# Kernel tuning notes

Hardware: AMD Instinct MI355X
Metric: run time of the kernel (lower is better)

## Reference

```python
import jax, jax.numpy as jnp
import numpy as np

# Uniform per-graph sizes (static shapes for jit):
B, M, P = 32, 40, 400          # graphs, ligand atoms/graph, protein nodes/graph
H, HEADS = 64, 8               # hid_dim, heads
E = B * M * P                  # total bipartite pairs = 512000


def _make_indices():
    """Replicates create_index() for uniform sizes: per-graph cartesian product."""
    g = np.arange(B, dtype=np.int64)
    # mol atom j of graph i repeated P times
    mol_index = np.repeat(np.arange(B * M, dtype=np.int64), P)
    # protein indices [i*P, (i+1)*P) tiled M times within each graph
    pro_index = (g[:, None, None] * P
                 + np.zeros((M, 1), dtype=np.int64)
                 + np.arange(P, dtype=np.int64)[None, None, :]).reshape(-1)
    mol_batch = np.repeat(g, M)   # create_batch(mol_size)
    return mol_index, pro_index, mol_batch


def setup_inputs() -> dict:
    key = jax.random.key(0)
    ks = jax.random.split(key, 8)
    mol_index, pro_index, mol_batch = _make_indices()
    s = 1.0 / np.sqrt(2 * H)
    return {
        "mol_feats": jax.random.normal(ks[0], (B * M, H), jnp.float32),
        "pro_feats": jax.random.normal(ks[1], (B * P, H), jnp.float32),
        "spatial_feats": jax.random.normal(ks[2], (B * P, H), jnp.float32),
        "mol_index": jnp.asarray(mol_index),
        "pro_index": jnp.asarray(pro_index),
        "mol_batch": jnp.asarray(mol_batch),
        "W_sigma": jax.random.normal(ks[3], (2 * H, HEADS), jnp.float32) * s,
        "b_sigma": jnp.zeros((HEADS,), jnp.float32),
        "W_mu": jax.random.normal(ks[4], (2 * H, HEADS), jnp.float32) * s,
        "b_mu": jnp.zeros((HEADS,), jnp.float32),
        "W1": jax.random.normal(ks[5], (HEADS, 2 * HEADS), jnp.float32) / np.sqrt(HEADS),
        "b1": jnp.zeros((2 * HEADS,), jnp.float32),
        "W2": jax.random.normal(ks[6], (2 * HEADS, 1), jnp.float32) / np.sqrt(2 * HEADS),
        "b2": jnp.zeros((1,), jnp.float32),
    }


def reference(mol_feats, pro_feats, spatial_feats, mol_index, pro_index, mol_batch,
              W_sigma, b_sigma, W_mu, b_mu, W1, b1, W2, b2):
    n_mol = mol_feats.shape[0]
    pro = pro_feats * spatial_feats                                  # [Np, H]
    # bipartite gather -> [E, 2H]
    atom_pairs = jnp.concatenate([mol_feats[mol_index], pro[pro_index]], axis=-1)
    sigma = jax.nn.elu(atom_pairs @ W_sigma + b_sigma) + 1.1         # [E, heads]
    mu = jax.nn.elu(atom_pairs @ W_mu + b_mu) + 1.0                  # [E, heads]
    # scatter_sum over mol atoms, then over graphs
    y = jax.ops.segment_sum(mu, mol_index, num_segments=n_mol)       # [Nm, heads]
    y = jax.ops.segment_sum(y, mol_batch, num_segments=B) * 0.001    # [B, heads]
    y = jax.nn.elu(y @ W1 + b1)
    y_pred = y @ W2 + b2                                             # [B, 1]
    return (mu, sigma, y_pred)
```

## Files before the change

### kernel.cpp

```cpp
#include <hip/hip_runtime.h>
#include <math.h>

#define B_   32
#define M_   40
#define P_   400
#define H_   64
#define HEADS_ 8
#define NMOL (B_ * M_)
#define NPRO (B_ * P_)
#define EPG  (M_ * P_)
#define E_   (B_ * EPG)
#define CHUNKS 63

__device__ __forceinline__ float elu_f(float x) {
    return x > 0.0f ? x : expm1f(x);
}

__global__ void precompute_kernel(const float* __restrict__ mol_feats,
                                  const float* __restrict__ pro_feats,
                                  const float* __restrict__ spatial,
                                  const float* __restrict__ Ws,
                                  const float* __restrict__ Wm,
                                  float* __restrict__ Amol_s, float* __restrict__ Amol_m,
                                  float* __restrict__ Apro_s, float* __restrict__ Apro_m)
{
    __shared__ float Wlds[2][128 * HEADS_];
    for (int i = threadIdx.x; i < 128 * HEADS_; i += 256) {
        Wlds[0][i] = Ws[i];
        Wlds[1][i] = Wm[i];
    }
    __syncthreads();

    const int o = threadIdx.x & 15;
    const int sel = o >> 3;
    const int h = o & 7;
    const int row = blockIdx.x * 16 + (threadIdx.x >> 4);
    if (row >= NMOL + NPRO) return;

    float acc = 0.0f;
    if (row < NMOL) {
        const float* f = mol_feats + row * H_;
        const float* w = &Wlds[sel][0 * HEADS_ + h];
        #pragma unroll
        for (int k = 0; k < H_; ++k) acc += f[k] * w[k * HEADS_];
        (sel ? Amol_m : Amol_s)[row * HEADS_ + h] = acc;
    } else {
        const int pr = row - NMOL;
        const float* pf = pro_feats + pr * H_;
        const float* sf = spatial   + pr * H_;
        const float* w = &Wlds[sel][H_ * HEADS_ + h];
        #pragma unroll
        for (int k = 0; k < H_; ++k) acc += pf[k] * sf[k] * w[k * HEADS_];
        (sel ? Apro_m : Apro_s)[pr * HEADS_ + h] = acc;
    }
}

__global__ void pair_kernel(const float* __restrict__ Amol_s, const float* __restrict__ Amol_m,
                            const float* __restrict__ Apro_s, const float* __restrict__ Apro_m,
                            const float* __restrict__ b_s, const float* __restrict__ b_m,
                            float* __restrict__ out_mu, float* __restrict__ out_sigma,
                            float* __restrict__ partials)
{
    const int g = blockIdx.x / CHUNKS;
    const int chunk = blockIdx.x - g * CHUNKS;
    const int el = chunk * 256 + threadIdx.x;

    float mu[HEADS_];
    #pragma unroll
    for (int h = 0; h < HEADS_; ++h) mu[h] = 0.0f;

    if (el < EPG) {
        const unsigned mr = (unsigned)el / P_;
        const unsigned p  = (unsigned)el - mr * P_;
        const int e = g * EPG + el;
        const int molrow = g * M_ + (int)mr;
        const int prorow = g * P_ + (int)p;

        const float4* ams = (const float4*)(Amol_s + molrow * HEADS_);
        const float4* amm = (const float4*)(Amol_m + molrow * HEADS_);
        const float4* aps = (const float4*)(Apro_s + prorow * HEADS_);
        const float4* apm = (const float4*)(Apro_m + prorow * HEADS_);

        float as[HEADS_], am[HEADS_];
        {
            float4 a0 = ams[0], a1 = ams[1], p0 = aps[0], p1 = aps[1];
            as[0]=a0.x+p0.x; as[1]=a0.y+p0.y; as[2]=a0.z+p0.z; as[3]=a0.w+p0.w;
            as[4]=a1.x+p1.x; as[5]=a1.y+p1.y; as[6]=a1.z+p1.z; as[7]=a1.w+p1.w;
        }
        {
            float4 a0 = amm[0], a1 = amm[1], p0 = apm[0], p1 = apm[1];
            am[0]=a0.x+p0.x; am[1]=a0.y+p0.y; am[2]=a0.z+p0.z; am[3]=a0.w+p0.w;
            am[4]=a1.x+p1.x; am[5]=a1.y+p1.y; am[6]=a1.z+p1.z; am[7]=a1.w+p1.w;
        }

        float sig[HEADS_];
        #pragma unroll
        for (int h = 0; h < HEADS_; ++h) {
            sig[h] = elu_f(as[h] + b_s[h]) + 1.1f;
            mu[h]  = elu_f(am[h] + b_m[h]) + 1.0f;
        }

        float4* oms = (float4*)(out_sigma + (size_t)e * HEADS_);
        float4* omm = (float4*)(out_mu    + (size_t)e * HEADS_);
        oms[0] = make_float4(sig[0], sig[1], sig[2], sig[3]);
        oms[1] = make_float4(sig[4], sig[5], sig[6], sig[7]);
        omm[0] = make_float4(mu[0], mu[1], mu[2], mu[3]);
        omm[1] = make_float4(mu[4], mu[5], mu[6], mu[7]);
    }

    const int lane = threadIdx.x & 63;
    const int wave = threadIdx.x >> 6;
    #pragma unroll
    for (int off = 32; off >= 1; off >>= 1) {
        #pragma unroll
        for (int h = 0; h < HEADS_; ++h)
            mu[h] += __shfl_down(mu[h], off, 64);
    }
    __shared__ float red[4][HEADS_];
    if (lane == 0) {
        #pragma unroll
        for (int h = 0; h < HEADS_; ++h) red[wave][h] = mu[h];
    }
    __syncthreads();
    if (threadIdx.x < HEADS_) {
        const int h = threadIdx.x;
        float s = red[0][h] + red[1][h] + red[2][h] + red[3][h];
        partials[(size_t)blockIdx.x * HEADS_ + h] = s;
    }
}

__global__ void final_kernel(const float* __restrict__ partials,
                             const float* __restrict__ W1, const float* __restrict__ b1,
                             const float* __restrict__ W2, const float* __restrict__ b2,
                             float* __restrict__ y_out)
{
    __shared__ float ys[B_][HEADS_];
    const int g = threadIdx.x >> 3;
    const int h = threadIdx.x & 7;
    if (g < B_) {
        float s = 0.0f;
        for (int c = 0; c < CHUNKS; ++c)
            s += partials[((size_t)g * CHUNKS + c) * HEADS_ + h];
        ys[g][h] = s * 0.001f;
    }
    __syncthreads();
    if (threadIdx.x < B_) {
        const int gg = threadIdx.x;
        float acc = b2[0];
        #pragma unroll
        for (int j = 0; j < 2 * HEADS_; ++j) {
            float hj = b1[j];
            #pragma unroll
            for (int k = 0; k < HEADS_; ++k)
                hj += ys[gg][k] * W1[k * (2 * HEADS_) + j];
            acc += elu_f(hj) * W2[j];
        }
        y_out[gg] = acc;
    }
}

extern "C" void kernel_launch(void* const* d_in, const int* in_sizes, int n_in,
                              void* d_out, int out_size, void* d_ws, size_t ws_size,
                              hipStream_t stream) {
    const float* mol_feats = (const float*)d_in[0];
    const float* pro_feats = (const float*)d_in[1];
    const float* spatial   = (const float*)d_in[2];
    const float* W_sigma = (const float*)d_in[6];
    const float* b_sigma = (const float*)d_in[7];
    const float* W_mu    = (const float*)d_in[8];
    const float* b_mu    = (const float*)d_in[9];
    const float* W1      = (const float*)d_in[10];
    const float* b1      = (const float*)d_in[11];
    const float* W2      = (const float*)d_in[12];
    const float* b2      = (const float*)d_in[13];

    float* out = (float*)d_out;
    float* out_mu    = out;
    float* out_sigma = out + (size_t)E_ * HEADS_;
    float* y_out     = out + 2 * (size_t)E_ * HEADS_;

    float* ws = (float*)d_ws;
    float* Amol_s = ws;
    float* Amol_m = Amol_s + NMOL * HEADS_;
    float* Apro_s = Amol_m + NMOL * HEADS_;
    float* Apro_m = Apro_s + NPRO * HEADS_;
    float* partials = Apro_m + NPRO * HEADS_;

    {
        const int rows = NMOL + NPRO;
        const int blocks = (rows + 15) / 16;
        precompute_kernel<<<blocks, 256, 0, stream>>>(
            mol_feats, pro_feats, spatial, W_sigma, W_mu,
            Amol_s, Amol_m, Apro_s, Apro_m);
    }
    pair_kernel<<<B_ * CHUNKS, 256, 0, stream>>>(
        Amol_s, Amol_m, Apro_s, Apro_m, b_sigma, b_mu,
        out_mu, out_sigma, partials);
    final_kernel<<<1, 256, 0, stream>>>(partials, W1, b1, W2, b2, y_out);
}
```

Measured before the change: 29.49 us.

## Process two pairs per thread, use exp2 ELU, vectorize precompute loads

The pair kernel now has each thread handle two consecutive pairs. This halves the block count and reuses the molecule-row loads and bias registers across both pairs. ELU uses exp2f in place of expm1f, with the +1 folded into the constant. The precompute kernel reads features as float4, and the final reduction loop is unrolled for the new chunk count. The cost is a strided store pattern across threads (each thread writes two adjacent 32-byte records), which may reduce store coalescing, and slightly less precision in ELU for small negative inputs.

```diff
diff --git a/kernel.cpp b/kernel.cpp
--- a/kernel.cpp
+++ b/kernel.cpp
@@ -10,10 +10,15 @@
 #define NPRO (B_ * P_)
 #define EPG  (M_ * P_)
 #define E_   (B_ * EPG)
-#define CHUNKS 63
+#define PPT  2
+#define BLOCK_PAIRS (256 * PPT)
+#define CHUNKS 32
+#define NBLK (B_ * CHUNKS)
+
+#define LOG2E 1.4426950408889634f
 
 __device__ __forceinline__ float elu_f(float x) {
-    return x > 0.0f ? x : expm1f(x);
+    return x > 0.0f ? x : exp2f(x * LOG2E) - 1.0f;
 }
 
 __global__ void precompute_kernel(const float* __restrict__ mol_feats,
@@ -39,18 +44,31 @@
 
     float acc = 0.0f;
     if (row < NMOL) {
-        const float* f = mol_feats + row * H_;
-        const float* w = &Wlds[sel][0 * HEADS_ + h];
-        #pragma unroll
-        for (int k = 0; k < H_; ++k) acc += f[k] * w[k * HEADS_];
+        const float4* f4 = (const float4*)(mol_feats + (size_t)row * H_);
+        const float* w = &Wlds[sel][h];
+        #pragma unroll
+        for (int kk = 0; kk < 16; ++kk) {
+            float4 v = f4[kk];
+            acc += v.x * w[(4 * kk + 0) * HEADS_]
+                 + v.y * w[(4 * kk + 1) * HEADS_]
+                 + v.z * w[(4 * kk + 2) * HEADS_]
+                 + v.w * w[(4 * kk + 3) * HEADS_];
+        }
         (sel ? Amol_m : Amol_s)[row * HEADS_ + h] = acc;
     } else {
         const int pr = row - NMOL;
-        const float* pf = pro_feats + pr * H_;
-        const float* sf = spatial   + pr * H_;
+        const float4* f4 = (const float4*)(pro_feats + (size_t)pr * H_);
+        const float4* s4 = (const float4*)(spatial   + (size_t)pr * H_);
         const float* w = &Wlds[sel][H_ * HEADS_ + h];
         #pragma unroll
-        for (int k = 0; k < H_; ++k) acc += pf[k] * sf[k] * w[k * HEADS_];
+        for (int kk = 0; kk < 16; ++kk) {
+            float4 v = f4[kk];
+            float4 s = s4[kk];
+            acc += (v.x * s.x) * w[(4 * kk + 0) * HEADS_]
+                 + (v.y * s.y) * w[(4 * kk + 1) * HEADS_]
+                 + (v.z * s.z) * w[(4 * kk + 2) * HEADS_]
+                 + (v.w * s.w) * w[(4 * kk + 3) * HEADS_];
+        }
         (sel ? Apro_m : Apro_s)[pr * HEADS_ + h] = acc;
     }
 }
@@ -61,71 +79,97 @@
                             float* __restrict__ out_mu, float* __restrict__ out_sigma,
                             float* __restrict__ partials)
 {
-    const int g = blockIdx.x / CHUNKS;
-    const int chunk = blockIdx.x - g * CHUNKS;
-    const int el = chunk * 256 + threadIdx.x;
-
-    float mu[HEADS_];
+    const int g = blockIdx.x >> 5;
+    const int chunk = blockIdx.x & 31;
+    const int t = threadIdx.x;
+
+    float bs[HEADS_], bm[HEADS_];
+    {
+        const float4* b4 = (const float4*)b_s;
+        float4 x0 = b4[0], x1 = b4[1];
+        bs[0]=x0.x; bs[1]=x0.y; bs[2]=x0.z; bs[3]=x0.w;
+        bs[4]=x1.x; bs[5]=x1.y; bs[6]=x1.z; bs[7]=x1.w;
+        const float4* c4 = (const float4*)b_m;
+        float4 y0 = c4[0], y1 = c4[1];
+        bm[0]=y0.x; bm[1]=y0.y; bm[2]=y0.z; bm[3]=y0.w;
+        bm[4]=y1.x; bm[5]=y1.y; bm[6]=y1.z; bm[7]=y1.w;
+    }
+
+    float acc[HEADS_];
     #pragma unroll
-    for (int h = 0; h < HEADS_; ++h) mu[h] = 0.0f;
-
+    for (int h = 0; h < HEADS_; ++h) acc[h] = 0.0f;
+
+    int el = chunk * BLOCK_PAIRS + t * PPT;
     if (el < EPG) {
-        const unsigned mr = (unsigned)el / P_;
-        const unsigned p  = (unsigned)el - mr * P_;
-        const int e = g * EPG + el;
-        const int molrow = g * M_ + (int)mr;
-        const int prorow = g * P_ + (int)p;
-
-        const float4* ams = (const float4*)(Amol_s + molrow * HEADS_);
-        const float4* amm = (const float4*)(Amol_m + molrow * HEADS_);
-        const float4* aps = (const float4*)(Apro_s + prorow * HEADS_);
-        const float4* apm = (const float4*)(Apro_m + prorow * HEADS_);
-
-        float as[HEADS_], am[HEADS_];
+        unsigned mr = (unsigned)el / P_;
+        unsigned p  = (unsigned)el - mr * P_;
+        const float* pro_s_base = Apro_s + (size_t)(g * P_) * HEADS_;
+        const float* pro_m_base = Apro_m + (size_t)(g * P_) * HEADS_;
+
+        float4 ms0, ms1, mm0, mm1;
         {
-            float4 a0 = ams[0], a1 = ams[1], p0 = aps[0], p1 = aps[1];
-            as[0]=a0.x+p0.x; as[1]=a0.y+p0.y; as[2]=a0.z+p0.z; as[3]=a0.w+p0.w;
-            as[4]=a1.x+p1.x; as[5]=a1.y+p1.y; as[6]=a1.z+p1.z; as[7]=a1.w+p1.w;
-        }
-        {
-            float4 a0 = amm[0], a1 = amm[1], p0 = apm[0], p1 = apm[1];
-            am[0]=a0.x+p0.x; am[1]=a0.y+p0.y; am[2]=a0.z+p0.z; am[3]=a0.w+p0.w;
-            am[4]=a1.x+p1.x; am[5]=a1.y+p1.y; am[6]=a1.z+p1.z; am[7]=a1.w+p1.w;
-        }
-
-        float sig[HEADS_];
-        #pragma unroll
-        for (int h = 0; h < HEADS_; ++h) {
-            sig[h] = elu_f(as[h] + b_s[h]) + 1.1f;
-            mu[h]  = elu_f(am[h] + b_m[h]) + 1.0f;
-        }
-
-        float4* oms = (float4*)(out_sigma + (size_t)e * HEADS_);
-        float4* omm = (float4*)(out_mu    + (size_t)e * HEADS_);
-        oms[0] = make_float4(sig[0], sig[1], sig[2], sig[3]);
-        oms[1] = make_float4(sig[4], sig[5], sig[6], sig[7]);
-        omm[0] = make_float4(mu[0], mu[1], mu[2], mu[3]);
-        omm[1] = make_float4(mu[4], mu[5], mu[6], mu[7]);
-    }
-
-    const int lane = threadIdx.x & 63;
-    const int wave = threadIdx.x >> 6;
+            const float4* a4 = (const float4*)(Amol_s + (size_t)(g * M_ + mr) * HEADS_);
+            const float4* c4 = (const float4*)(Amol_m + (size_t)(g * M_ + mr) * HEADS_);
+            ms0 = a4[0]; ms1 = a4[1]; mm0 = c4[0]; mm1 = c4[1];
+        }
+
+        #pragma unroll
+        for (int j = 0; j < PPT; ++j) {
+            const float4* ps4 = (const float4*)(pro_s_base + (size_t)p * HEADS_);
+            const float4* pm4 = (const float4*)(pro_m_base + (size_t)p * HEADS_);
+            float4 p0 = ps4[0], p1 = ps4[1], q0 = pm4[0], q1 = pm4[1];
+
+            float xs[HEADS_], xm[HEADS_];
+            xs[0]=ms0.x+p0.x; xs[1]=ms0.y+p0.y; xs[2]=ms0.z+p0.z; xs[3]=ms0.w+p0.w;
+            xs[4]=ms1.x+p1.x; xs[5]=ms1.y+p1.y; xs[6]=ms1.z+p1.z; xs[7]=ms1.w+p1.w;
+            xm[0]=mm0.x+q0.x; xm[1]=mm0.y+q0.y; xm[2]=mm0.z+q0.z; xm[3]=mm0.w+q0.w;
+            xm[4]=mm1.x+q1.x; xm[5]=mm1.y+q1.y; xm[6]=mm1.z+q1.z; xm[7]=mm1.w+q1.w;
+
+            float sig[HEADS_], mu[HEADS_];
+            #pragma unroll
+            for (int h = 0; h < HEADS_; ++h) {
+                float x = xs[h] + bs[h];
+                sig[h] = x > 0.0f ? x + 1.1f : exp2f(x * LOG2E) + 0.1f;
+                float y = xm[h] + bm[h];
+                mu[h] = y > 0.0f ? y + 1.0f : exp2f(y * LOG2E);
+                acc[h] += mu[h];
+            }
+
+            const size_t e = (size_t)(g * EPG + el + j);
+            float4* oms = (float4*)(out_sigma + e * HEADS_);
+            float4* omm = (float4*)(out_mu    + e * HEADS_);
+            oms[0] = make_float4(sig[0], sig[1], sig[2], sig[3]);
+            oms[1] = make_float4(sig[4], sig[5], sig[6], sig[7]);
+            omm[0] = make_float4(mu[0], mu[1], mu[2], mu[3]);
+            omm[1] = make_float4(mu[4], mu[5], mu[6], mu[7]);
+
+            ++p;
+            if (p == P_) {
+                p = 0; ++mr;
+                const float4* a4 = (const float4*)(Amol_s + (size_t)(g * M_ + mr) * HEADS_);
+                const float4* c4 = (const float4*)(Amol_m + (size_t)(g * M_ + mr) * HEADS_);
+                ms0 = a4[0]; ms1 = a4[1]; mm0 = c4[0]; mm1 = c4[1];
+            }
+        }
+    }
+
+    const int lane = t & 63;
+    const int wave = t >> 6;
     #pragma unroll
     for (int off = 32; off >= 1; off >>= 1) {
         #pragma unroll
         for (int h = 0; h < HEADS_; ++h)
-            mu[h] += __shfl_down(mu[h], off, 64);
+            acc[h] += __shfl_down(acc[h], off, 64);
     }
     __shared__ float red[4][HEADS_];
     if (lane == 0) {
         #pragma unroll
-        for (int h = 0; h < HEADS_; ++h) red[wave][h] = mu[h];
+        for (int h = 0; h < HEADS_; ++h) red[wave][h] = acc[h];
     }
     __syncthreads();
-    if (threadIdx.x < HEADS_) {
-        const int h = threadIdx.x;
-        float s = red[0][h] + red[1][h] + red[2][h] + red[3][h];
-        partials[(size_t)blockIdx.x * HEADS_ + h] = s;
+    if (t < HEADS_) {
+        float s = red[0][t] + red[1][t] + red[2][t] + red[3][t];
+        partials[(size_t)blockIdx.x * HEADS_ + t] = s;
     }
 }
 
@@ -137,25 +181,26 @@
     __shared__ float ys[B_][HEADS_];
     const int g = threadIdx.x >> 3;
     const int h = threadIdx.x & 7;
-    if (g < B_) {
+    {
         float s = 0.0f;
+        #pragma unroll
         for (int c = 0; c < CHUNKS; ++c)
-            s += partials[((size_t)g * CHUNKS + c) * HEADS_ + h];
+            s += partials[(size_t)((g << 5) + c) * HEADS_ + h];
         ys[g][h] = s * 0.001f;
     }
     __syncthreads();
     if (threadIdx.x < B_) {
         const int gg = threadIdx.x;
-        float acc = b2[0];
+        float accy = b2[0];
         #pragma unroll
         for (int j = 0; j < 2 * HEADS_; ++j) {
             float hj = b1[j];
             #pragma unroll
             for (int k = 0; k < HEADS_; ++k)
                 hj += ys[gg][k] * W1[k * (2 * HEADS_) + j];
-            acc += elu_f(hj) * W2[j];
-        }
-        y_out[gg] = acc;
+            accy += elu_f(hj) * W2[j];
+        }
+        y_out[gg] = accy;
     }
 }
 
@@ -193,7 +238,7 @@
             mol_feats, pro_feats, spatial, W_sigma, W_mu,
             Amol_s, Amol_m, Apro_s, Apro_m);
     }
-    pair_kernel<<<B_ * CHUNKS, 256, 0, stream>>>(
+    pair_kernel<<<NBLK, 256, 0, stream>>>(
         Amol_s, Amol_m, Apro_s, Apro_m, b_sigma, b_mu,
         out_mu, out_sigma, partials);
     final_kernel<<<1, 256, 0, stream>>>(partials, W1, b1, W2, b2, y_out);
```

Measured after the change: 30.00 us. About the same (+1.7%).
